# Kernel tuning notes

Measured on AMD Instinct MI355X. Metric: run time of the kernel, lower is better.

The kernel has to match this reference:

```python
import jax, jax.numpy as jnp
import numpy as np

TOP_K = 2
NORM_TOPK_PROB = True


def setup_inputs() -> dict:
    key = jax.random.key(0)
    k1, k2 = jax.random.split(key)
    hidden_states = jax.random.normal(k1, (4, 4096, 2048), dtype=jnp.float32)
    # gate weight [n_routed_experts, hidden_size], kaiming-uniform-like scale
    weight = jax.random.normal(k2, (64, 2048), dtype=jnp.float32) * 0.02
    return {"hidden_states": hidden_states, "weight": weight}


def reference(hidden_states, weight):
    bsz, seq_len, h = hidden_states.shape
    x = hidden_states.reshape(-1, h)                      # [T, H]
    logits = jnp.einsum("th,eh->te", x, weight)           # [T, E]
    scores = jax.nn.softmax(logits, axis=-1)              # [T, E]
    topk_weight, topk_idx = jax.lax.top_k(scores, TOP_K)  # [T, K] each
    if TOP_K > 1 and NORM_TOPK_PROB:
        topk_weight = topk_weight / (topk_weight.sum(axis=-1, keepdims=True) + 1e-20)
    return (topk_idx.reshape(bsz, seq_len, -1), topk_weight.reshape(bsz, seq_len, -1))
```

## Files before the change

kernel.cpp:

```cpp
#include <hip/hip_runtime.h>
#include <math.h>

#define H    2048
#define NE   64
#define TOKB 64
#define KC   64
#define NCH  32
#define NBUF 4
#define TAU  4.0e-3f
#define NEGF (-3.0e38f)

typedef __bf16 bf16x8 __attribute__((ext_vector_type(8)));
typedef float  f32x16 __attribute__((ext_vector_type(16)));

#define MFMA(a, b, c) __builtin_amdgcn_mfma_f32_32x32x16_bf16((a), (b), (c), 0, 0, 0)
#define LD4(p) (*reinterpret_cast<const float4*>(p))

__device__ __forceinline__ void cvt8(const float4 a, const float4 b,
                                     bf16x8& hi, bf16x8& lo) {
    const float v0 = a.x, v1 = a.y, v2 = a.z, v3 = a.w;
    const float v4 = b.x, v5 = b.y, v6 = b.z, v7 = b.w;
    hi[0] = (__bf16)v0; lo[0] = (__bf16)(v0 - (float)hi[0]);
    hi[1] = (__bf16)v1; lo[1] = (__bf16)(v1 - (float)hi[1]);
    hi[2] = (__bf16)v2; lo[2] = (__bf16)(v2 - (float)hi[2]);
    hi[3] = (__bf16)v3; lo[3] = (__bf16)(v3 - (float)hi[3]);
    hi[4] = (__bf16)v4; lo[4] = (__bf16)(v4 - (float)hi[4]);
    hi[5] = (__bf16)v5; lo[5] = (__bf16)(v5 - (float)hi[5]);
    hi[6] = (__bf16)v6; lo[6] = (__bf16)(v6 - (float)hi[6]);
    hi[7] = (__bf16)v7; lo[7] = (__bf16)(v7 - (float)hi[7]);
}

__device__ __forceinline__ void gll16(const void* g, void* l) {
    __builtin_amdgcn_global_load_lds(
        (const __attribute__((address_space(1))) void*)g,
        (__attribute__((address_space(3))) void*)l, 16, 0, 0);
}

__global__ __launch_bounds__(256) void prep_w(
    const float* __restrict__ w, __bf16* __restrict__ wp, int* __restrict__ wl)
{
    const int e   = blockIdx.x;
    const int tid = threadIdx.x;
    if (e == 0 && tid == 0) wl[0] = 0;
    const float4 a = LD4(&w[e * H + tid * 8]);
    const float4 b = LD4(&w[e * H + tid * 8 + 4]);
    bf16x8 hi, lo;
    cvt8(a, b, hi, lo);
    const int c  = tid >> 2;
    const int kk = (tid & 3) * 8;
    *reinterpret_cast<bf16x8*>(wp + e * 4096 + c * 64 + kk)      = hi;
    *reinterpret_cast<bf16x8*>(wp + e * 4096 + c * 64 + 32 + kk) = lo;
}

__global__ __launch_bounds__(512) void moe_gate_mfma(
    const float* __restrict__ x,
    const __bf16* __restrict__ wp,
    float* __restrict__ out, int woff,
    int* __restrict__ wl, int wlcap)
{
    extern __shared__ char lds[];

    const int tid  = threadIdx.x;
    const int lane = tid & 63;
    const int wv   = tid >> 6;
    const int mt   = wv >> 2;
    const int kq   = wv & 3;
    const int lo5  = lane & 31;
    const int hi5  = lane >> 5;
    const int t0   = blockIdx.x * TOKB;

    const char* sbase[4];
    #pragma unroll
    for (int s = 0; s < 4; ++s) {
        const int byte = ((wv * 4 + s) * 64 + lane) * 16;
        if (byte < 16384) {
            const int row = byte >> 8;
            const int sl  = ((byte >> 4) & 15) ^ (row & 15);
            sbase[s] = (const char*)wp + (size_t)row * 8192 + sl * 16;
        } else {
            const int b   = byte - 16384;
            const int row = b >> 8;
            const int sl  = ((b >> 4) & 15) ^ (row & 15);
            sbase[s] = (const char*)x + (size_t)(t0 + row) * 8192 + sl * 16;
        }
    }

    f32x16 acc0, acc1;
    #pragma unroll
    for (int i = 0; i < 16; ++i) { acc0[i] = 0.f; acc1[i] = 0.f; }

    #pragma unroll
    for (int p = 0; p < 3; ++p)
        #pragma unroll
        for (int s = 0; s < 4; ++s)
            gll16(sbase[s] + p * 256, lds + p * 32768 + ((wv * 4 + s) * 64) * 16);

    const int sa  = (kq >> 1) * 8 + (kq & 1) * 2 + hi5;
    const int ra0 = lo5, ra1 = 32 + lo5;
    const int offAh0 = ra0 * 256 + (((sa)     ^ (ra0 & 15)) << 4);
    const int offAl0 = ra0 * 256 + (((sa + 4) ^ (ra0 & 15)) << 4);
    const int offAh1 = ra1 * 256 + (((sa)     ^ (ra1 & 15)) << 4);
    const int offAl1 = ra1 * 256 + (((sa + 4) ^ (ra1 & 15)) << 4);
    const int rb  = mt * 32 + lo5;
    const int sb  = kq * 4 + hi5 * 2;
    const int offB0 = 16384 + rb * 256 + (((sb)     ^ (rb & 15)) << 4);
    const int offB1 = 16384 + rb * 256 + (((sb + 1) ^ (rb & 15)) << 4);

    for (int c = 0; c < NCH; ++c) {
        if (c < NCH - 2) {
            asm volatile("s_waitcnt vmcnt(8)" ::: "memory");
        } else if (c == NCH - 2) {
            asm volatile("s_waitcnt vmcnt(4)" ::: "memory");
        } else {
            asm volatile("s_waitcnt vmcnt(0)" ::: "memory");
        }
        __builtin_amdgcn_s_barrier();

        const char* bufb = lds + (c & 3) * 32768;
        const bf16x8 ah0 = *reinterpret_cast<const bf16x8*>(bufb + offAh0);
        const bf16x8 al0 = *reinterpret_cast<const bf16x8*>(bufb + offAl0);
        const bf16x8 ah1 = *reinterpret_cast<const bf16x8*>(bufb + offAh1);
        const bf16x8 al1 = *reinterpret_cast<const bf16x8*>(bufb + offAl1);
        const float4 b1  = *reinterpret_cast<const float4*>(bufb + offB0);
        const float4 b2  = *reinterpret_cast<const float4*>(bufb + offB1);

        bf16x8 bh, bl;
        cvt8(b1, b2, bh, bl);

        if (c + 3 < NCH) {
            #pragma unroll
            for (int s = 0; s < 4; ++s)
                gll16(sbase[s] + (c + 3) * 256,
                      lds + ((c + 3) & 3) * 32768 + ((wv * 4 + s) * 64) * 16);
        }

        acc0 = MFMA(ah0, bh, acc0);
        acc1 = MFMA(ah1, bh, acc1);
        acc0 = MFMA(ah0, bl, acc0);
        acc1 = MFMA(ah1, bl, acc1);
        acc0 = MFMA(al0, bh, acc0);
        acc1 = MFMA(al1, bh, acc1);
    }

    __syncthreads();
    float* S = reinterpret_cast<float*>(lds);
    if (kq != 0) {
        const int base = ((mt * 3 + (kq - 1)) * 32 + lo5) * 65;
        #pragma unroll
        for (int r = 0; r < 16; ++r) {
            const int e0 = (r & 3) + 8 * (r >> 2) + 4 * hi5;
            S[base + e0]      = acc0[r];
            S[base + 32 + e0] = acc1[r];
        }
    }
    __syncthreads();
    if (kq != 0) return;
    #pragma unroll
    for (int q = 0; q < 3; ++q) {
        const int base = ((mt * 3 + q) * 32 + lo5) * 65;
        #pragma unroll
        for (int r = 0; r < 16; ++r) {
            const int e0 = (r & 3) + 8 * (r >> 2) + 4 * hi5;
            acc0[r] += S[base + e0];
            acc1[r] += S[base + 32 + e0];
        }
    }

    float m1 = NEGF, m2 = NEGF, m3 = NEGF;
    int   i1 = 0, i2 = 0;
    #pragma unroll
    for (int r = 0; r < 16; ++r) {
        const float v = acc0[r];
        const int   e = (r & 3) + 8 * (r >> 2) + 4 * hi5;
        if (v > m1)      { m3 = m2; m2 = m1; i2 = i1; m1 = v; i1 = e; }
        else if (v > m2) { m3 = m2; m2 = v; i2 = e; }
        else if (v > m3) { m3 = v; }
    }
    #pragma unroll
    for (int r = 0; r < 16; ++r) {
        const float v = acc1[r];
        const int   e = 32 + (r & 3) + 8 * (r >> 2) + 4 * hi5;
        if (v > m1)      { m3 = m2; m2 = m1; i2 = i1; m1 = v; i1 = e; }
        else if (v > m2) { m3 = m2; m2 = v; i2 = e; }
        else if (v > m3) { m3 = v; }
    }

    const float n1 = __shfl_xor(m1, 32), n2 = __shfl_xor(m2, 32), n3 = __shfl_xor(m3, 32);
    const int   j1 = __shfl_xor(i1, 32), j2 = __shfl_xor(i2, 32);

    float a1, a2, a3, b1, b2, b3; int ia1, ia2, ib1, ib2;
    const bool aF = (m1 > n1) || (m1 == n1 && i1 < j1);
    if (aF) { a1=m1; a2=m2; a3=m3; ia1=i1; ia2=i2; b1=n1; b2=n2; b3=n3; ib1=j1; ib2=j2; }
    else    { a1=n1; a2=n2; a3=n3; ia1=j1; ia2=j2; b1=m1; b2=m2; b3=m3; ib1=i1; ib2=i2; }

    const float o1 = a1; const int oi1 = ia1;
    float o2, o3; int oi2;
    const bool a2F = (a2 > b1) || (a2 == b1 && ia2 < ib1);
    if (a2F) { o2 = a2; oi2 = ia2; o3 = (a3 > b1) ? a3 : b1; }
    else     { o2 = b1; oi2 = ib1; o3 = (a2 > b2) ? a2 : b2; }

    if (hi5 == 0) {
        const int t = t0 + mt * 32 + lo5;
        const float r = expf(o2 - o1);
        const float s = 1.0f + r;
        out[2 * t + 0]        = (float)oi1;
        out[2 * t + 1]        = (float)oi2;
        out[woff + 2 * t + 0] = 1.0f / s;
        out[woff + 2 * t + 1] = r / s;
        if ((o1 - o2 < TAU) || (o2 - o3 < TAU)) {
            const int pos = atomicAdd(wl, 1);
            if (pos < wlcap) wl[1 + pos] = t;
        }
    }
}

__global__ __launch_bounds__(256) void moe_refine_fp64(
    const float* __restrict__ x, const float* __restrict__ w,
    float* __restrict__ out, int woff,
    const int* __restrict__ wl, int wlcap)
{
    __shared__ double Sd[3][NE];
    const int lane = threadIdx.x & 63;
    const int wv   = threadIdx.x >> 6;
    const int ks   = wv * 512;
    int cnt = wl[0];
    if (cnt > wlcap) cnt = wlcap;

    for (int i = blockIdx.x; i < cnt; i += gridDim.x) {
        const int t = wl[1 + i];

        const float4 xa = LD4(&x[(size_t)t * H + ks + lane * 4]);
        const float4 xb = LD4(&x[(size_t)t * H + ks + 256 + lane * 4]);
        const double x0 = xa.x, x1 = xa.y, x2 = xa.z, x3 = xa.w;
        const double x4 = xb.x, x5 = xb.y, x6 = xb.z, x7 = xb.w;

        double myacc = 0.0;
        #pragma unroll 4
        for (int e = 0; e < NE; ++e) {
            const float4 wa = LD4(&w[(size_t)e * H + ks + lane * 4]);
            const float4 wb = LD4(&w[(size_t)e * H + ks + 256 + lane * 4]);
            double sA = 0.0, sB = 0.0;
            sA = fma((double)wa.x, x0, sA); sA = fma((double)wa.y, x1, sA);
            sA = fma((double)wa.z, x2, sA); sA = fma((double)wa.w, x3, sA);
            sB = fma((double)wb.x, x4, sB); sB = fma((double)wb.y, x5, sB);
            sB = fma((double)wb.z, x6, sB); sB = fma((double)wb.w, x7, sB);
            double s = sA + sB;
            #pragma unroll
            for (int off = 1; off < 64; off <<= 1)
                s += __shfl_xor(s, off);
            if (lane == e) myacc = s;
        }

        if (wv > 0) Sd[wv - 1][lane] = myacc;
        __syncthreads();
        if (wv == 0) {
            const double acc = ((myacc + Sd[0][lane]) + Sd[1][lane]) + Sd[2][lane];

            double v = acc; int bi = lane;
            #pragma unroll
            for (int off = 32; off > 0; off >>= 1) {
                double ov = __shfl_xor(v, off);
                int    oi = __shfl_xor(bi, off);
                if (ov > v || (ov == v && oi < bi)) { v = ov; bi = oi; }
            }
            const double m1 = v; const int i1 = bi;

            double v2 = (lane == i1) ? -1.0e300 : acc; int b2 = lane;
            #pragma unroll
            for (int off = 32; off > 0; off >>= 1) {
                double ov = __shfl_xor(v2, off);
                int    oi = __shfl_xor(b2, off);
                if (ov > v2 || (ov == v2 && oi < b2)) { v2 = ov; b2 = oi; }
            }
            const double m2 = v2; const int i2 = b2;

            if (lane == 0) {
                const double r = exp(m2 - m1);
                const double s = 1.0 + r;
                out[2 * t + 0]        = (float)i1;
                out[2 * t + 1]        = (float)i2;
                out[woff + 2 * t + 0] = (float)(1.0 / s);
                out[woff + 2 * t + 1] = (float)(r / s);
            }
        }
        __syncthreads();
    }
}

extern "C" void kernel_launch(void* const* d_in, const int* in_sizes, int n_in,
                              void* d_out, int out_size, void* d_ws, size_t ws_size,
                              hipStream_t stream) {
    const float* x   = (const float*)d_in[0];
    const float* wgt = (const float*)d_in[1];
    float* out = (float*)d_out;

    const int T    = in_sizes[0] / H;
    const int woff = out_size / 2;

    int*    wl = (int*)d_ws;
    __bf16* wp = (__bf16*)((char*)d_ws + 131072);
    int wlcap = T;

    (void)hipFuncSetAttribute((const void*)moe_gate_mfma,
                              hipFuncAttributeMaxDynamicSharedMemorySize, 131072);

    prep_w<<<dim3(NE), dim3(256), 0, stream>>>(wgt, wp, wl);

    moe_gate_mfma<<<dim3(T / TOKB), dim3(512), 131072, stream>>>(
        x, wp, out, woff, wl, wlcap);

    moe_refine_fp64<<<dim3(512), dim3(256), 0, stream>>>(
        x, wgt, out, woff, wl, wlcap);
}
```

Before: 60.78 us.

## Stream weights from global into registers and double the K chunk per stage

The weight operand is now pre-laid out in an MFMA-fragment-friendly order and read directly from global (L2-cached) into registers each chunk, instead of staged through LDS. This frees the whole LDS ring for activation tiles, so each chunk covers 128 K elements instead of 64, halving the number of barrier/wait iterations. The cost is per-iteration global loads of weights whose latency is not hidden by the LDS pipeline, plus more registers for the extra fragments.

```diff
diff --git a/kernel.cpp b/kernel.cpp
--- a/kernel.cpp
+++ b/kernel.cpp
@@ -4,8 +4,8 @@
 #define H    2048
 #define NE   64
 #define TOKB 64
-#define KC   64
-#define NCH  32
+#define KC   128
+#define NCH  16
 #define NBUF 4
 #define TAU  4.0e-3f
 #define NEGF (-3.0e38f)
@@ -46,10 +46,11 @@
     const float4 b = LD4(&w[e * H + tid * 8 + 4]);
     bf16x8 hi, lo;
     cvt8(a, b, hi, lo);
-    const int c  = tid >> 2;
-    const int kk = (tid & 3) * 8;
-    *reinterpret_cast<bf16x8*>(wp + e * 4096 + c * 64 + kk)      = hi;
-    *reinterpret_cast<bf16x8*>(wp + e * 4096 + c * 64 + 32 + kk) = lo;
+    const int g  = tid >> 1;
+    const int kh = tid & 1;
+    char* base = (char*)wp + (size_t)g * 4096 + kh * 1024 + e * 16;
+    *reinterpret_cast<bf16x8*>(base)        = hi;
+    *reinterpret_cast<bf16x8*>(base + 2048) = lo;
 }
 
 __global__ __launch_bounds__(512) void moe_gate_mfma(
@@ -71,18 +72,12 @@
 
     const char* sbase[4];
     #pragma unroll
-    for (int s = 0; s < 4; ++s) {
-        const int byte = ((wv * 4 + s) * 64 + lane) * 16;
-        if (byte < 16384) {
-            const int row = byte >> 8;
-            const int sl  = ((byte >> 4) & 15) ^ (row & 15);
-            sbase[s] = (const char*)wp + (size_t)row * 8192 + sl * 16;
-        } else {
-            const int b   = byte - 16384;
-            const int row = b >> 8;
-            const int sl  = ((b >> 4) & 15) ^ (row & 15);
-            sbase[s] = (const char*)x + (size_t)(t0 + row) * 8192 + sl * 16;
-        }
+    for (int q = 0; q < 4; ++q) {
+        const int idx16 = q * 512 + tid;
+        const int row   = idx16 >> 5;
+        const int sl    = idx16 & 31;
+        sbase[q] = (const char*)x + (size_t)(t0 + row) * 8192
+                   + ((sl ^ (row & 31)) * 16);
     }
 
     f32x16 acc0, acc1;
@@ -92,19 +87,19 @@
     #pragma unroll
     for (int p = 0; p < 3; ++p)
         #pragma unroll
-        for (int s = 0; s < 4; ++s)
-            gll16(sbase[s] + p * 256, lds + p * 32768 + ((wv * 4 + s) * 64) * 16);
-
-    const int sa  = (kq >> 1) * 8 + (kq & 1) * 2 + hi5;
-    const int ra0 = lo5, ra1 = 32 + lo5;
-    const int offAh0 = ra0 * 256 + (((sa)     ^ (ra0 & 15)) << 4);
-    const int offAl0 = ra0 * 256 + (((sa + 4) ^ (ra0 & 15)) << 4);
-    const int offAh1 = ra1 * 256 + (((sa)     ^ (ra1 & 15)) << 4);
-    const int offAl1 = ra1 * 256 + (((sa + 4) ^ (ra1 & 15)) << 4);
+        for (int q = 0; q < 4; ++q)
+            gll16(sbase[q] + p * 512, lds + p * 32768 + (q * 512 + wv * 64) * 16);
+
     const int rb  = mt * 32 + lo5;
-    const int sb  = kq * 4 + hi5 * 2;
-    const int offB0 = 16384 + rb * 256 + (((sb)     ^ (rb & 15)) << 4);
-    const int offB1 = 16384 + rb * 256 + (((sb + 1) ^ (rb & 15)) << 4);
+    const int rbk = rb & 31;
+    const int sb0 = kq * 8 + hi5 * 2;
+    const int sb1 = kq * 8 + 4 + hi5 * 2;
+    const int offB00 = rb * 512 + (((sb0)     ^ rbk) << 4);
+    const int offB01 = rb * 512 + (((sb0 + 1) ^ rbk) << 4);
+    const int offB10 = rb * 512 + (((sb1)     ^ rbk) << 4);
+    const int offB11 = rb * 512 + (((sb1 + 1) ^ rbk) << 4);
+
+    const char* wpb = (const char*)wp + hi5 * 1024 + lo5 * 16;
 
     for (int c = 0; c < NCH; ++c) {
         if (c < NCH - 2) {
@@ -116,30 +111,45 @@
         }
         __builtin_amdgcn_s_barrier();
 
+        const char* wg = wpb + (size_t)(c * 8 + kq * 2) * 4096;
+        const bf16x8 ah0a = *reinterpret_cast<const bf16x8*>(wg);
+        const bf16x8 ah1a = *reinterpret_cast<const bf16x8*>(wg + 512);
+        const bf16x8 al0a = *reinterpret_cast<const bf16x8*>(wg + 2048);
+        const bf16x8 al1a = *reinterpret_cast<const bf16x8*>(wg + 2560);
+        const bf16x8 ah0b = *reinterpret_cast<const bf16x8*>(wg + 4096);
+        const bf16x8 ah1b = *reinterpret_cast<const bf16x8*>(wg + 4608);
+        const bf16x8 al0b = *reinterpret_cast<const bf16x8*>(wg + 6144);
+        const bf16x8 al1b = *reinterpret_cast<const bf16x8*>(wg + 6656);
+
         const char* bufb = lds + (c & 3) * 32768;
-        const bf16x8 ah0 = *reinterpret_cast<const bf16x8*>(bufb + offAh0);
-        const bf16x8 al0 = *reinterpret_cast<const bf16x8*>(bufb + offAl0);
-        const bf16x8 ah1 = *reinterpret_cast<const bf16x8*>(bufb + offAh1);
-        const bf16x8 al1 = *reinterpret_cast<const bf16x8*>(bufb + offAl1);
-        const float4 b1  = *reinterpret_cast<const float4*>(bufb + offB0);
-        const float4 b2  = *reinterpret_cast<const float4*>(bufb + offB1);
-
-        bf16x8 bh, bl;
-        cvt8(b1, b2, bh, bl);
+        const float4 b00 = *reinterpret_cast<const float4*>(bufb + offB00);
+        const float4 b01 = *reinterpret_cast<const float4*>(bufb + offB01);
+        const float4 b10 = *reinterpret_cast<const float4*>(bufb + offB10);
+        const float4 b11 = *reinterpret_cast<const float4*>(bufb + offB11);
 
         if (c + 3 < NCH) {
             #pragma unroll
-            for (int s = 0; s < 4; ++s)
-                gll16(sbase[s] + (c + 3) * 256,
-                      lds + ((c + 3) & 3) * 32768 + ((wv * 4 + s) * 64) * 16);
-        }
-
-        acc0 = MFMA(ah0, bh, acc0);
-        acc1 = MFMA(ah1, bh, acc1);
-        acc0 = MFMA(ah0, bl, acc0);
-        acc1 = MFMA(ah1, bl, acc1);
-        acc0 = MFMA(al0, bh, acc0);
-        acc1 = MFMA(al1, bh, acc1);
+            for (int q = 0; q < 4; ++q)
+                gll16(sbase[q] + (c + 3) * 512,
+                      lds + ((c + 3) & 3) * 32768 + (q * 512 + wv * 64) * 16);
+        }
+
+        bf16x8 bh0, bl0, bh1, bl1;
+        cvt8(b00, b01, bh0, bl0);
+        cvt8(b10, b11, bh1, bl1);
+
+        acc0 = MFMA(ah0a, bh0, acc0);
+        acc1 = MFMA(ah1a, bh0, acc1);
+        acc0 = MFMA(ah0a, bl0, acc0);
+        acc1 = MFMA(ah1a, bl0, acc1);
+        acc0 = MFMA(al0a, bh0, acc0);
+        acc1 = MFMA(al1a, bh0, acc1);
+        acc0 = MFMA(ah0b, bh1, acc0);
+        acc1 = MFMA(ah1b, bh1, acc1);
+        acc0 = MFMA(ah0b, bl1, acc0);
+        acc1 = MFMA(ah1b, bl1, acc1);
+        acc0 = MFMA(al0b, bh1, acc0);
+        acc1 = MFMA(al1b, bh1, acc1);
     }
 
     __syncthreads();
```

After: 67.58 us. 11.2% more time.

## Split K across all eight waves and reuse weight fragments over two token tiles

Applied to the files above, without the earlier changes.

Changes the work split so each of the eight waves owns a K slice and computes both 32-token tiles, instead of two token tiles times four K quarters. The pre-packed weight layout changes so each wave reads its hi/lo weight fragments once per 256-wide window and reuses them for two x chunks. x is streamed through a 4-slot ring and the weights through a double buffer, with finer waitcnt/barrier staging. The aim is less LDS and weight traffic per MFMA, at the cost of an eight-way cross-wave reduction, more accumulator registers and more LDS.

```diff
diff --git a/kernel.cpp b/kernel.cpp
--- a/kernel.cpp
+++ b/kernel.cpp
@@ -4,9 +4,6 @@
 #define H    2048
 #define NE   64
 #define TOKB 64
-#define KC   64
-#define NCH  32
-#define NBUF 4
 #define TAU  4.0e-3f
 #define NEGF (-3.0e38f)
 
@@ -46,15 +43,15 @@
     const float4 b = LD4(&w[e * H + tid * 8 + 4]);
     bf16x8 hi, lo;
     cvt8(a, b, hi, lo);
-    const int c  = tid >> 2;
-    const int kk = (tid & 3) * 8;
-    *reinterpret_cast<bf16x8*>(wp + e * 4096 + c * 64 + kk)      = hi;
-    *reinterpret_cast<bf16x8*>(wp + e * 4096 + c * 64 + 32 + kk) = lo;
+    const int g  = tid >> 1;
+    const int kh = tid & 1;
+    char* base = (char*)wp + (size_t)g * 4096 + kh * 1024 + e * 16;
+    *reinterpret_cast<bf16x8*>(base)        = hi;
+    *reinterpret_cast<bf16x8*>(base + 2048) = lo;
 }
 
 __global__ __launch_bounds__(512) void moe_gate_mfma(
-    const float* __restrict__ x,
-    const __bf16* __restrict__ wp,
+    const float* __restrict__ x, const __bf16* __restrict__ wp,
     float* __restrict__ out, int woff,
     int* __restrict__ wl, int wlcap)
 {
@@ -62,154 +59,179 @@
 
     const int tid  = threadIdx.x;
     const int lane = tid & 63;
-    const int wv   = tid >> 6;
-    const int mt   = wv >> 2;
-    const int kq   = wv & 3;
+    const int kq   = tid >> 6;
     const int lo5  = lane & 31;
     const int hi5  = lane >> 5;
     const int t0   = blockIdx.x * TOKB;
 
-    const char* sbase[4];
+    char* Xr = lds + 65536;
+
+    const int u0 = (kq * 2 + 0) * 64 + lane;
+    const int u1 = (kq * 2 + 1) * 64 + lane;
+    const char* xb  = (const char*)x;
+    const char* wpb = (const char*)wp;
+    const size_t xo0 = (size_t)(t0 + (u0 >> 5)) * 8192 + (((u0 & 31) ^ (u0 >> 5)) << 4);
+    const size_t xo1 = (size_t)(t0 + (u1 >> 5)) * 8192 + (((u1 & 31) ^ (u1 >> 5)) << 4);
+
+    f32x16 a00, a10, a01, a11;
     #pragma unroll
-    for (int s = 0; s < 4; ++s) {
-        const int byte = ((wv * 4 + s) * 64 + lane) * 16;
-        if (byte < 16384) {
-            const int row = byte >> 8;
-            const int sl  = ((byte >> 4) & 15) ^ (row & 15);
-            sbase[s] = (const char*)wp + (size_t)row * 8192 + sl * 16;
-        } else {
-            const int b   = byte - 16384;
-            const int row = b >> 8;
-            const int sl  = ((b >> 4) & 15) ^ (row & 15);
-            sbase[s] = (const char*)x + (size_t)(t0 + row) * 8192 + sl * 16;
-        }
-    }
-
-    f32x16 acc0, acc1;
-    #pragma unroll
-    for (int i = 0; i < 16; ++i) { acc0[i] = 0.f; acc1[i] = 0.f; }
-
-    #pragma unroll
-    for (int p = 0; p < 3; ++p)
-        #pragma unroll
-        for (int s = 0; s < 4; ++s)
-            gll16(sbase[s] + p * 256, lds + p * 32768 + ((wv * 4 + s) * 64) * 16);
-
-    const int sa  = (kq >> 1) * 8 + (kq & 1) * 2 + hi5;
-    const int ra0 = lo5, ra1 = 32 + lo5;
-    const int offAh0 = ra0 * 256 + (((sa)     ^ (ra0 & 15)) << 4);
-    const int offAl0 = ra0 * 256 + (((sa + 4) ^ (ra0 & 15)) << 4);
-    const int offAh1 = ra1 * 256 + (((sa)     ^ (ra1 & 15)) << 4);
-    const int offAl1 = ra1 * 256 + (((sa + 4) ^ (ra1 & 15)) << 4);
-    const int rb  = mt * 32 + lo5;
-    const int sb  = kq * 4 + hi5 * 2;
-    const int offB0 = 16384 + rb * 256 + (((sb)     ^ (rb & 15)) << 4);
-    const int offB1 = 16384 + rb * 256 + (((sb + 1) ^ (rb & 15)) << 4);
-
-    for (int c = 0; c < NCH; ++c) {
-        if (c < NCH - 2) {
-            asm volatile("s_waitcnt vmcnt(8)" ::: "memory");
-        } else if (c == NCH - 2) {
-            asm volatile("s_waitcnt vmcnt(4)" ::: "memory");
-        } else {
-            asm volatile("s_waitcnt vmcnt(0)" ::: "memory");
-        }
+    for (int i = 0; i < 16; ++i) { a00[i]=0.f; a10[i]=0.f; a01[i]=0.f; a11[i]=0.f; }
+
+    gll16(wpb +         u0*16, lds +         u0*16);
+    gll16(wpb +         u1*16, lds +         u1*16);
+    gll16(wpb + 16384 + u0*16, lds + 16384 + u0*16);
+    gll16(wpb + 16384 + u1*16, lds + 16384 + u1*16);
+    gll16(xb + xo0,            Xr + 0*16384 + u0*16);
+    gll16(xb + xo1,            Xr + 0*16384 + u1*16);
+    gll16(xb + xo0 + 262144,   Xr + 1*16384 + u0*16);
+    gll16(xb + xo1 + 262144,   Xr + 1*16384 + u1*16);
+    gll16(xb + xo0 + 512,      Xr + 2*16384 + u0*16);
+    gll16(xb + xo1 + 512,      Xr + 2*16384 + u1*16);
+
+    const int s0  = kq * 4 + hi5 * 2;
+    const int xr0 = lo5 * 512 + (((s0)     ^ lo5) << 4);
+    const int xr1 = lo5 * 512 + (((s0 + 1) ^ lo5) << 4);
+    const int wfA = kq * 4096 + hi5 * 1024 + lo5 * 16;
+
+    for (int win = 0; win < 16; ++win) {
+        const int rA = (2 * win) & 3;
+        const int rB = (rA + 1) & 3;
+        const int wS = (rA + 3) & 3;
+        const char* wb = lds + (win & 1) * 32768;
+
+        if (win < 15) { asm volatile("s_waitcnt vmcnt(4)" ::: "memory"); }
+        else          { asm volatile("s_waitcnt vmcnt(2)" ::: "memory"); }
         __builtin_amdgcn_s_barrier();
-
-        const char* bufb = lds + (c & 3) * 32768;
-        const bf16x8 ah0 = *reinterpret_cast<const bf16x8*>(bufb + offAh0);
-        const bf16x8 al0 = *reinterpret_cast<const bf16x8*>(bufb + offAl0);
-        const bf16x8 ah1 = *reinterpret_cast<const bf16x8*>(bufb + offAh1);
-        const bf16x8 al1 = *reinterpret_cast<const bf16x8*>(bufb + offAl1);
-        const float4 b1  = *reinterpret_cast<const float4*>(bufb + offB0);
-        const float4 b2  = *reinterpret_cast<const float4*>(bufb + offB1);
-
-        bf16x8 bh, bl;
-        cvt8(b1, b2, bh, bl);
-
-        if (c + 3 < NCH) {
-            #pragma unroll
-            for (int s = 0; s < 4; ++s)
-                gll16(sbase[s] + (c + 3) * 256,
-                      lds + ((c + 3) & 3) * 32768 + ((wv * 4 + s) * 64) * 16);
-        }
-
-        acc0 = MFMA(ah0, bh, acc0);
-        acc1 = MFMA(ah1, bh, acc1);
-        acc0 = MFMA(ah0, bl, acc0);
-        acc1 = MFMA(ah1, bl, acc1);
-        acc0 = MFMA(al0, bh, acc0);
-        acc1 = MFMA(al1, bh, acc1);
+        if (win < 15) {
+            const size_t wno = (size_t)(win + 1) * 32768;
+            char* wd = lds + ((win + 1) & 1) * 32768;
+            gll16(wpb + wno +         u0*16, wd +         u0*16);
+            gll16(wpb + wno +         u1*16, wd +         u1*16);
+            gll16(wpb + wno + 16384 + u0*16, wd + 16384 + u0*16);
+            gll16(wpb + wno + 16384 + u1*16, wd + 16384 + u1*16);
+            const size_t xoff = 262144 + (size_t)(win + 1) * 512;
+            gll16(xb + xo0 + xoff, Xr + wS*16384 + u0*16);
+            gll16(xb + xo1 + xoff, Xr + wS*16384 + u1*16);
+        }
+        {
+            const char* xbuf = Xr + rA * 16384;
+            const bf16x8 ah0 = *reinterpret_cast<const bf16x8*>(wb + wfA);
+            const bf16x8 al0 = *reinterpret_cast<const bf16x8*>(wb + wfA + 2048);
+            const bf16x8 ah1 = *reinterpret_cast<const bf16x8*>(wb + wfA + 512);
+            const bf16x8 al1 = *reinterpret_cast<const bf16x8*>(wb + wfA + 2560);
+            const float4 b1  = *reinterpret_cast<const float4*>(xbuf + xr0);
+            const float4 b2  = *reinterpret_cast<const float4*>(xbuf + xr1);
+            bf16x8 bh, bl;
+            cvt8(b1, b2, bh, bl);
+            a00 = MFMA(ah0, bh, a00);  a10 = MFMA(ah1, bh, a10);
+            a00 = MFMA(ah0, bl, a00);  a10 = MFMA(ah1, bl, a10);
+            a00 = MFMA(al0, bh, a00);  a10 = MFMA(al1, bh, a10);
+        }
+
+        if (win < 15) { asm volatile("s_waitcnt vmcnt(8)" ::: "memory"); }
+        else          { asm volatile("s_waitcnt vmcnt(0)" ::: "memory"); }
+        __builtin_amdgcn_s_barrier();
+        if (win < 14) {
+            const size_t xoff = (size_t)(win + 2) * 512;
+            gll16(xb + xo0 + xoff, Xr + rA*16384 + u0*16);
+            gll16(xb + xo1 + xoff, Xr + rA*16384 + u1*16);
+        }
+        {
+            const char* xbuf = Xr + rB * 16384;
+            const bf16x8 ah0 = *reinterpret_cast<const bf16x8*>(wb + wfA);
+            const bf16x8 al0 = *reinterpret_cast<const bf16x8*>(wb + wfA + 2048);
+            const bf16x8 ah1 = *reinterpret_cast<const bf16x8*>(wb + wfA + 512);
+            const bf16x8 al1 = *reinterpret_cast<const bf16x8*>(wb + wfA + 2560);
+            const float4 b1  = *reinterpret_cast<const float4*>(xbuf + xr0);
+            const float4 b2  = *reinterpret_cast<const float4*>(xbuf + xr1);
+            bf16x8 bh, bl;
+            cvt8(b1, b2, bh, bl);
+            a01 = MFMA(ah0, bh, a01);  a11 = MFMA(ah1, bh, a11);
+            a01 = MFMA(ah0, bl, a01);  a11 = MFMA(ah1, bl, a11);
+            a01 = MFMA(al0, bh, a01);  a11 = MFMA(al1, bh, a11);
+        }
     }
 
     __syncthreads();
     float* S = reinterpret_cast<float*>(lds);
     if (kq != 0) {
-        const int base = ((mt * 3 + (kq - 1)) * 32 + lo5) * 65;
         #pragma unroll
         for (int r = 0; r < 16; ++r) {
             const int e0 = (r & 3) + 8 * (r >> 2) + 4 * hi5;
-            S[base + e0]      = acc0[r];
-            S[base + 32 + e0] = acc1[r];
+            const int b0 = ((kq - 1) * 64 +      lo5) * 65;
+            const int b1 = ((kq - 1) * 64 + 32 + lo5) * 65;
+            S[b0 + e0]      = a00[r];
+            S[b0 + 32 + e0] = a10[r];
+            S[b1 + e0]      = a01[r];
+            S[b1 + 32 + e0] = a11[r];
         }
     }
     __syncthreads();
     if (kq != 0) return;
     #pragma unroll
-    for (int q = 0; q < 3; ++q) {
-        const int base = ((mt * 3 + q) * 32 + lo5) * 65;
+    for (int q = 1; q < 8; ++q) {
         #pragma unroll
         for (int r = 0; r < 16; ++r) {
             const int e0 = (r & 3) + 8 * (r >> 2) + 4 * hi5;
-            acc0[r] += S[base + e0];
-            acc1[r] += S[base + 32 + e0];
-        }
-    }
-
-    float m1 = NEGF, m2 = NEGF, m3 = NEGF;
-    int   i1 = 0, i2 = 0;
+            const int b0 = ((q - 1) * 64 +      lo5) * 65;
+            const int b1 = ((q - 1) * 64 + 32 + lo5) * 65;
+            a00[r] += S[b0 + e0];
+            a10[r] += S[b0 + 32 + e0];
+            a01[r] += S[b1 + e0];
+            a11[r] += S[b1 + 32 + e0];
+        }
+    }
+
     #pragma unroll
-    for (int r = 0; r < 16; ++r) {
-        const float v = acc0[r];
-        const int   e = (r & 3) + 8 * (r >> 2) + 4 * hi5;
-        if (v > m1)      { m3 = m2; m2 = m1; i2 = i1; m1 = v; i1 = e; }
-        else if (v > m2) { m3 = m2; m2 = v; i2 = e; }
-        else if (v > m3) { m3 = v; }
-    }
-    #pragma unroll
-    for (int r = 0; r < 16; ++r) {
-        const float v = acc1[r];
-        const int   e = 32 + (r & 3) + 8 * (r >> 2) + 4 * hi5;
-        if (v > m1)      { m3 = m2; m2 = m1; i2 = i1; m1 = v; i1 = e; }
-        else if (v > m2) { m3 = m2; m2 = v; i2 = e; }
-        else if (v > m3) { m3 = v; }
-    }
-
-    const float n1 = __shfl_xor(m1, 32), n2 = __shfl_xor(m2, 32), n3 = __shfl_xor(m3, 32);
-    const int   j1 = __shfl_xor(i1, 32), j2 = __shfl_xor(i2, 32);
-
-    float a1, a2, a3, b1, b2, b3; int ia1, ia2, ib1, ib2;
-    const bool aF = (m1 > n1) || (m1 == n1 && i1 < j1);
-    if (aF) { a1=m1; a2=m2; a3=m3; ia1=i1; ia2=i2; b1=n1; b2=n2; b3=n3; ib1=j1; ib2=j2; }
-    else    { a1=n1; a2=n2; a3=n3; ia1=j1; ia2=j2; b1=m1; b2=m2; b3=m3; ib1=i1; ib2=i2; }
-
-    const float o1 = a1; const int oi1 = ia1;
-    float o2, o3; int oi2;
-    const bool a2F = (a2 > b1) || (a2 == b1 && ia2 < ib1);
-    if (a2F) { o2 = a2; oi2 = ia2; o3 = (a3 > b1) ? a3 : b1; }
-    else     { o2 = b1; oi2 = ib1; o3 = (a2 > b2) ? a2 : b2; }
-
-    if (hi5 == 0) {
-        const int t = t0 + mt * 32 + lo5;
-        const float r = expf(o2 - o1);
-        const float s = 1.0f + r;
-        out[2 * t + 0]        = (float)oi1;
-        out[2 * t + 1]        = (float)oi2;
-        out[woff + 2 * t + 0] = 1.0f / s;
-        out[woff + 2 * t + 1] = r / s;
-        if ((o1 - o2 < TAU) || (o2 - o3 < TAU)) {
-            const int pos = atomicAdd(wl, 1);
-            if (pos < wlcap) wl[1 + pos] = t;
+    for (int g = 0; g < 2; ++g) {
+        const f32x16& A0 = (g == 0) ? a00 : a01;
+        const f32x16& A1 = (g == 0) ? a10 : a11;
+
+        float m1 = NEGF, m2 = NEGF, m3 = NEGF;
+        int   i1 = 0, i2 = 0;
+        #pragma unroll
+        for (int r = 0; r < 16; ++r) {
+            const float v = A0[r];
+            const int   e = (r & 3) + 8 * (r >> 2) + 4 * hi5;
+            if (v > m1)      { m3 = m2; m2 = m1; i2 = i1; m1 = v; i1 = e; }
+            else if (v > m2) { m3 = m2; m2 = v; i2 = e; }
+            else if (v > m3) { m3 = v; }
+        }
+        #pragma unroll
+        for (int r = 0; r < 16; ++r) {
+            const float v = A1[r];
+            const int   e = 32 + (r & 3) + 8 * (r >> 2) + 4 * hi5;
+            if (v > m1)      { m3 = m2; m2 = m1; i2 = i1; m1 = v; i1 = e; }
+            else if (v > m2) { m3 = m2; m2 = v; i2 = e; }
+            else if (v > m3) { m3 = v; }
+        }
+
+        const float n1 = __shfl_xor(m1, 32), n2 = __shfl_xor(m2, 32), n3 = __shfl_xor(m3, 32);
+        const int   j1 = __shfl_xor(i1, 32), j2 = __shfl_xor(i2, 32);
+
+        float c1, c2, c3, d1, d2, d3; int ic1, ic2, id1, id2;
+        const bool aF = (m1 > n1) || (m1 == n1 && i1 < j1);
+        if (aF) { c1=m1; c2=m2; c3=m3; ic1=i1; ic2=i2; d1=n1; d2=n2; d3=n3; id1=j1; id2=j2; }
+        else    { c1=n1; c2=n2; c3=n3; ic1=j1; ic2=j2; d1=m1; d2=m2; d3=m3; id1=i1; id2=i2; }
+
+        const float o1 = c1; const int oi1 = ic1;
+        float o2, o3; int oi2;
+        const bool c2F = (c2 > d1) || (c2 == d1 && ic2 < id1);
+        if (c2F) { o2 = c2; oi2 = ic2; o3 = (c3 > d1) ? c3 : d1; }
+        else     { o2 = d1; oi2 = id1; o3 = (c2 > d2) ? c2 : d2; }
+
+        if (hi5 == 0) {
+            const int t = t0 + g * 32 + lo5;
+            const float r = expf(o2 - o1);
+            const float s = 1.0f + r;
+            out[2 * t + 0]        = (float)oi1;
+            out[2 * t + 1]        = (float)oi2;
+            out[woff + 2 * t + 0] = 1.0f / s;
+            out[woff + 2 * t + 1] = r / s;
+            if ((o1 - o2 < TAU) || (o2 - o3 < TAU)) {
+                const int pos = atomicAdd(wl, 1);
+                if (pos < wlcap) wl[1 + pos] = t;
+            }
         }
     }
 }
```

New measurement: 109.7 us. +80.5%, slower.

## Replace direct global-to-LDS loads with register-staged double-buffered prefetch

Applied to the files above, without the earlier changes.

Global loads no longer go straight into LDS through global_load_lds. Each chunk is now loaded into registers two chunks ahead, alternating between two register sets, and written to LDS after the MFMAs for the current chunk. The main loop is fully unrolled and uses sched_barrier to fix the instruction order. This trades the async LDS-load path and its vmcnt waits for extra VGPRs and explicit ds_write traffic. Because each LDS store must wait for its global load, the loop may stall more often.

```diff
diff --git a/kernel.cpp b/kernel.cpp
--- a/kernel.cpp
+++ b/kernel.cpp
@@ -6,7 +6,6 @@
 #define TOKB 64
 #define KC   64
 #define NCH  32
-#define NBUF 4
 #define TAU  4.0e-3f
 #define NEGF (-3.0e38f)
 
@@ -28,12 +27,6 @@
     hi[5] = (__bf16)v5; lo[5] = (__bf16)(v5 - (float)hi[5]);
     hi[6] = (__bf16)v6; lo[6] = (__bf16)(v6 - (float)hi[6]);
     hi[7] = (__bf16)v7; lo[7] = (__bf16)(v7 - (float)hi[7]);
-}
-
-__device__ __forceinline__ void gll16(const void* g, void* l) {
-    __builtin_amdgcn_global_load_lds(
-        (const __attribute__((address_space(1))) void*)g,
-        (__attribute__((address_space(3))) void*)l, 16, 0, 0);
 }
 
 __global__ __launch_bounds__(256) void prep_w(
@@ -69,10 +62,11 @@
     const int hi5  = lane >> 5;
     const int t0   = blockIdx.x * TOKB;
 
-    const char* sbase[4];
+    const char* sbase[4]; int ldd[4];
     #pragma unroll
     for (int s = 0; s < 4; ++s) {
         const int byte = ((wv * 4 + s) * 64 + lane) * 16;
+        ldd[s] = byte;
         if (byte < 16384) {
             const int row = byte >> 8;
             const int sl  = ((byte >> 4) & 15) ^ (row & 15);
@@ -89,11 +83,18 @@
     #pragma unroll
     for (int i = 0; i < 16; ++i) { acc0[i] = 0.f; acc1[i] = 0.f; }
 
-    #pragma unroll
-    for (int p = 0; p < 3; ++p)
-        #pragma unroll
-        for (int s = 0; s < 4; ++s)
-            gll16(sbase[s] + p * 256, lds + p * 32768 + ((wv * 4 + s) * 64) * 16);
+    float4 rgA[4], rgB[4];
+
+    #pragma unroll
+    for (int s = 0; s < 4; ++s) rgA[s] = LD4(sbase[s]);
+    #pragma unroll
+    for (int s = 0; s < 4; ++s) rgB[s] = LD4(sbase[s] + 256);
+    __builtin_amdgcn_sched_barrier(0);
+    #pragma unroll
+    for (int s = 0; s < 4; ++s)
+        *reinterpret_cast<float4*>(lds + ldd[s]) = rgA[s];
+    asm volatile("s_waitcnt lgkmcnt(0)" ::: "memory");
+    __builtin_amdgcn_s_barrier();
 
     const int sa  = (kq >> 1) * 8 + (kq & 1) * 2 + hi5;
     const int ra0 = lo5, ra1 = 32 + lo5;
@@ -106,17 +107,22 @@
     const int offB0 = 16384 + rb * 256 + (((sb)     ^ (rb & 15)) << 4);
     const int offB1 = 16384 + rb * 256 + (((sb + 1) ^ (rb & 15)) << 4);
 
+    #pragma unroll
     for (int c = 0; c < NCH; ++c) {
-        if (c < NCH - 2) {
-            asm volatile("s_waitcnt vmcnt(8)" ::: "memory");
-        } else if (c == NCH - 2) {
-            asm volatile("s_waitcnt vmcnt(4)" ::: "memory");
-        } else {
-            asm volatile("s_waitcnt vmcnt(0)" ::: "memory");
-        }
-        __builtin_amdgcn_s_barrier();
-
-        const char* bufb = lds + (c & 3) * 32768;
+        if (c + 2 < NCH) {
+            if ((c & 1) == 0) {
+                #pragma unroll
+                for (int s = 0; s < 4; ++s)
+                    rgA[s] = LD4(sbase[s] + (size_t)(c + 2) * 256);
+            } else {
+                #pragma unroll
+                for (int s = 0; s < 4; ++s)
+                    rgB[s] = LD4(sbase[s] + (size_t)(c + 2) * 256);
+            }
+        }
+        __builtin_amdgcn_sched_barrier(0);
+
+        const char* bufb = lds + (size_t)(c & 3) * 32768;
         const bf16x8 ah0 = *reinterpret_cast<const bf16x8*>(bufb + offAh0);
         const bf16x8 al0 = *reinterpret_cast<const bf16x8*>(bufb + offAl0);
         const bf16x8 ah1 = *reinterpret_cast<const bf16x8*>(bufb + offAh1);
@@ -126,20 +132,27 @@
 
         bf16x8 bh, bl;
         cvt8(b1, b2, bh, bl);
-
-        if (c + 3 < NCH) {
-            #pragma unroll
-            for (int s = 0; s < 4; ++s)
-                gll16(sbase[s] + (c + 3) * 256,
-                      lds + ((c + 3) & 3) * 32768 + ((wv * 4 + s) * 64) * 16);
-        }
-
         acc0 = MFMA(ah0, bh, acc0);
         acc1 = MFMA(ah1, bh, acc1);
         acc0 = MFMA(ah0, bl, acc0);
         acc1 = MFMA(ah1, bl, acc1);
         acc0 = MFMA(al0, bh, acc0);
         acc1 = MFMA(al1, bh, acc1);
+
+        if (c + 1 < NCH) {
+            char* dst = lds + (size_t)((c + 1) & 3) * 32768;
+            if ((c & 1) == 0) {
+                #pragma unroll
+                for (int s = 0; s < 4; ++s)
+                    *reinterpret_cast<float4*>(dst + ldd[s]) = rgB[s];
+            } else {
+                #pragma unroll
+                for (int s = 0; s < 4; ++s)
+                    *reinterpret_cast<float4*>(dst + ldd[s]) = rgA[s];
+            }
+        }
+        asm volatile("s_waitcnt lgkmcnt(0)" ::: "memory");
+        __builtin_amdgcn_s_barrier();
     }
 
     __syncthreads();
```

New measurement: 118.5 us. 95.0% more time.
